# Performance work log

Hardware: AMD Instinct MI355X
Metric: run time of the kernel (lower is better)

The kernel has to match this reference:

```python
import jax, jax.numpy as jnp
import numpy as np

DIM = 768
HEADS = 12
HEAD_DIM = DIM // HEADS
SCALE = HEAD_DIM ** -0.5
ALPHA = 0.1


def setup_inputs() -> dict:
    key = jax.random.key(0)
    ks = jax.random.split(key, 6)
    B, N, C = 16, 577, DIM
    x = jax.random.normal(ks[0], (B, N, C), dtype=jnp.float32)
    attn_weight = jax.random.uniform(ks[1], (B, N - 1), dtype=jnp.float32)
    w_qkv = jax.random.normal(ks[2], (C, 3 * C), dtype=jnp.float32) * (C ** -0.5)
    b_qkv = jnp.zeros((3 * C,), dtype=jnp.float32)
    w_proj = jax.random.normal(ks[3], (C, C), dtype=jnp.float32) * (C ** -0.5)
    b_proj = jnp.zeros((C,), dtype=jnp.float32)
    return {"x": x, "attn_weight": attn_weight, "w_qkv": w_qkv, "b_qkv": b_qkv,
            "w_proj": w_proj, "b_proj": b_proj}


def reference(x, attn_weight, w_qkv, b_qkv, w_proj, b_proj):
    B, N, C = x.shape
    H, D = HEADS, HEAD_DIM
    qkv = (x @ w_qkv + b_qkv).reshape(B, N, 3, H, D)
    qkv = jnp.transpose(qkv, (2, 0, 3, 1, 4))  # [3, B, H, N, D]
    q, k, v = qkv[0], qkv[1], qkv[2]
    attn = jnp.einsum('bhnd,bhmd->bhnm', q, k) * SCALE  # [B,H,N,N]
    patch_attn = attn[:, :, 0, 1:]  # pre-softmax CLS->patch scores
    # reweight CLS row (excluding CLS->CLS) before softmax
    w = attn_weight[:, None, None, :]  # [B,1,1,N-1]
    cls_row = attn[:, :, 0:1, 1:] * (w * ALPHA + (1.0 - ALPHA))
    attn = attn.at[:, :, 0:1, 1:].set(cls_row)
    attn = jax.nn.softmax(attn, axis=-1)
    out = jnp.einsum('bhnm,bhmd->bhnd', attn, v)
    out = jnp.transpose(out, (0, 2, 1, 3)).reshape(B, N, C)
    out = out @ w_proj + b_proj
    return out, patch_attn
```

## Files before the change

kernel.cpp:

```cpp
#include <hip/hip_runtime.h>
#include <hip/hip_bf16.h>
#include <math.h>

#define B_    16
#define N_    577
#define C_    768
#define H_    12
#define D_    64
#define M_    (B_ * N_)
#define MP_   9344
#define QKVN  2304
#define NP_   640
#define SCALE 0.125f
#define ALPHA 0.1f
#define OUT0  (B_ * N_ * C_)

#define NB_CONV 7008
#define NB_T1   1728
#define NB_T2   576

typedef __attribute__((ext_vector_type(8))) short short8;
typedef __attribute__((ext_vector_type(4))) float f32x4;
typedef __hip_bfloat16 bf16;

__device__ __forceinline__ float exp2fast(float x) {
    return __builtin_amdgcn_exp2f(x);
}

__device__ __forceinline__ void load16(const void* g, void* l) {
    __builtin_amdgcn_global_load_lds(
        (const __attribute__((address_space(1))) unsigned int*)g,
        (__attribute__((address_space(3))) unsigned int*)l, 16, 0, 0);
}

__device__ __forceinline__ f32x4 mfma16(short8 a, short8 b, f32x4 c) {
    return __builtin_amdgcn_mfma_f32_16x16x32_bf16(a, b, c, 0, 0, 0);
}

#define FENCE() asm volatile("" ::: "memory")
#define BARRIER() do { FENCE(); __builtin_amdgcn_s_barrier(); FENCE(); } while (0)
#define WAITLGKM0() asm volatile("s_waitcnt lgkmcnt(0)" ::: "memory")

__global__ __launch_bounds__(256) void prep(const float* __restrict__ x,
                                            bf16* __restrict__ xb,
                                            const float* __restrict__ wq,
                                            bf16* __restrict__ wqT,
                                            const float* __restrict__ wp,
                                            bf16* __restrict__ wpT) {
    __shared__ float tile[32][33];
    const int bid = blockIdx.x;
    if (bid < NB_CONV) {
        int idx = bid * 256 + threadIdx.x;
        int m = idx / 192;
        bf16 tmp[4];
        if (m < M_) {
            float4 f = ((const float4*)x)[idx];
            tmp[0] = __float2bfloat16(f.x);
            tmp[1] = __float2bfloat16(f.y);
            tmp[2] = __float2bfloat16(f.z);
            tmp[3] = __float2bfloat16(f.w);
        } else {
            tmp[0] = tmp[1] = tmp[2] = tmp[3] = __float2bfloat16(0.f);
        }
        ((ushort4*)xb)[idx] = *(ushort4*)tmp;
        return;
    }
    const float* src; bf16* dst; int C, R, bx, by;
    if (bid < NB_CONV + NB_T1) {
        int r = bid - NB_CONV;
        bx = r % 72; by = r / 72; src = wq; dst = wqT; R = 768; C = QKVN;
    } else {
        int r = bid - NB_CONV - NB_T1;
        bx = r % 24; by = r / 24; src = wp; dst = wpT; R = 768; C = 768;
    }
    int cb = bx * 32, rb = by * 32;
    int tx = threadIdx.x & 31, ty = threadIdx.x >> 5;
    #pragma unroll
    for (int i = 0; i < 32; i += 8)
        tile[ty + i][tx] = src[(size_t)(rb + ty + i) * C + cb + tx];
    __syncthreads();
    #pragma unroll
    for (int i = 0; i < 32; i += 8)
        dst[(size_t)(cb + ty + i) * R + rb + tx] = __float2bfloat16(tile[tx][ty + i]);
}

__global__ __launch_bounds__(512, 2) void gemm256(const bf16* __restrict__ A,
                                                  const bf16* __restrict__ BT,
                                                  const float* __restrict__ bias,
                                                  bf16* __restrict__ q,
                                                  bf16* __restrict__ kk,
                                                  bf16* __restrict__ vt,
                                                  float* __restrict__ out,
                                                  int mode, int nby) {
    __shared__ __align__(16) char smem[131072];

    const int bid = blockIdx.x;
    const int mb = bid / nby;
    const int nb = bid % nby;
    const int m0 = mb * 256, n0 = nb * 256;
    const int t = threadIdx.x, lane = t & 63, w = t >> 6;
    const int wr = w >> 2, wc = w & 3;
    const int r16 = lane & 15, quad = lane >> 4;

    f32x4 acc[8][4];
    #pragma unroll
    for (int i = 0; i < 8; i++)
        #pragma unroll
        for (int j = 0; j < 4; j++) acc[i][j] = (f32x4)(0.f);

    const int lrow = lane >> 3;
    const int clog = ((lane & 7) ^ lrow) << 4;
    const int s2 = w * 2;
    const char* gA = (const char*)A  + (size_t)(m0 + lrow) * 1536 + clog;
    const char* gB = (const char*)BT + (size_t)(n0 + lrow) * 1536 + clog;

    auto stA = [&](int kt2, int half) {
        int ro = (half * 128 + s2 * 8) * 1536 + kt2 * 128;
        char* d = (char*)smem + (kt2 & 1) * 32768 + half * 16384 + s2 * 1024;
        load16(gA + ro, d);
        load16(gA + ro + 8 * 1536, d + 1024);
    };
    auto stB = [&](int kt2, int half) {
        int ro = (half * 128 + s2 * 8) * 1536 + kt2 * 128;
        char* d = (char*)smem + 65536 + (kt2 & 1) * 32768 + half * 16384 + s2 * 1024;
        load16(gB + ro, d);
        load16(gB + ro + 8 * 1536, d + 1024);
    };

    stA(0, 0); stA(0, 1); stB(0, 0); stB(0, 1);
    stA(1, 0); stA(1, 1);
    asm volatile("s_waitcnt vmcnt(4)" ::: "memory");
    BARRIER();

    const int sw = r16 & 7;
    const int g0 = (quad ^ sw) << 4;
    const int g1 = ((quad ^ 4) ^ sw) << 4;

    short8 af0[8], af1[8], bq0[2], bq1[2];

    #pragma unroll
    for (int kt = 0; kt < 12; kt++) {
        const int cur = kt & 1;
        const char* Ap = (const char*)smem + cur * 32768 + (wr * 128 + r16) * 128;
        const char* Bp = (const char*)smem + 65536 + cur * 32768 + (wc * 64 + r16) * 128;

        #pragma unroll
        for (int mi = 0; mi < 8; mi++) af0[mi] = *(const short8*)(Ap + mi * 2048 + g0);
        bq0[0] = *(const short8*)(Bp + 0 * 2048 + g0);
        bq0[1] = *(const short8*)(Bp + 1 * 2048 + g0);
        if (kt < 11) stB(kt + 1, 0);
        BARRIER();
        WAITLGKM0();
        __builtin_amdgcn_s_setprio(1);
        #pragma unroll
        for (int mi = 0; mi < 8; mi++) acc[mi][0] = mfma16(af0[mi], bq0[0], acc[mi][0]);
        #pragma unroll
        for (int mi = 0; mi < 8; mi++) acc[mi][1] = mfma16(af0[mi], bq0[1], acc[mi][1]);
        __builtin_amdgcn_s_setprio(0);
        BARRIER();

        #pragma unroll
        for (int mi = 0; mi < 8; mi++) af1[mi] = *(const short8*)(Ap + mi * 2048 + g1);
        bq1[0] = *(const short8*)(Bp + 2 * 2048 + g0);
        bq1[1] = *(const short8*)(Bp + 3 * 2048 + g0);
        if (kt < 11) stB(kt + 1, 1);
        BARRIER();
        WAITLGKM0();
        __builtin_amdgcn_s_setprio(1);
        #pragma unroll
        for (int mi = 0; mi < 8; mi++) acc[mi][2] = mfma16(af0[mi], bq1[0], acc[mi][2]);
        #pragma unroll
        for (int mi = 0; mi < 8; mi++) acc[mi][3] = mfma16(af0[mi], bq1[1], acc[mi][3]);
        __builtin_amdgcn_s_setprio(0);
        BARRIER();

        bq0[0] = *(const short8*)(Bp + 0 * 2048 + g1);
        bq0[1] = *(const short8*)(Bp + 1 * 2048 + g1);
        if (kt < 10) stA(kt + 2, 0);
        BARRIER();
        WAITLGKM0();
        __builtin_amdgcn_s_setprio(1);
        #pragma unroll
        for (int mi = 0; mi < 8; mi++) acc[mi][0] = mfma16(af1[mi], bq0[0], acc[mi][0]);
        #pragma unroll
        for (int mi = 0; mi < 8; mi++) acc[mi][1] = mfma16(af1[mi], bq0[1], acc[mi][1]);
        __builtin_amdgcn_s_setprio(0);
        BARRIER();

        bq1[0] = *(const short8*)(Bp + 2 * 2048 + g1);
        bq1[1] = *(const short8*)(Bp + 3 * 2048 + g1);
        if (kt < 10) stA(kt + 2, 1);
        BARRIER();
        WAITLGKM0();
        __builtin_amdgcn_s_setprio(1);
        #pragma unroll
        for (int mi = 0; mi < 8; mi++) acc[mi][2] = mfma16(af1[mi], bq1[0], acc[mi][2]);
        #pragma unroll
        for (int mi = 0; mi < 8; mi++) acc[mi][3] = mfma16(af1[mi], bq1[1], acc[mi][3]);
        __builtin_amdgcn_s_setprio(0);
        if (kt < 10) { asm volatile("s_waitcnt vmcnt(4)" ::: "memory"); }
        else         { asm volatile("s_waitcnt vmcnt(0)" ::: "memory"); }
        BARRIER();
    }

    float bs[4];
    #pragma unroll
    for (int nj = 0; nj < 4; nj++) bs[nj] = bias[n0 + wc * 64 + nj * 16 + r16];

    if (mode == 1) {
        #pragma unroll
        for (int mi = 0; mi < 8; mi++) {
            #pragma unroll
            for (int nj = 0; nj < 4; nj++) {
                #pragma unroll
                for (int r = 0; r < 4; r++) {
                    int m = m0 + wr * 128 + mi * 16 + quad * 4 + r;
                    if (m >= M_) continue;
                    out[(size_t)m * 768 + n0 + wc * 64 + nj * 16 + r16] = acc[mi][nj][r] + bs[nj];
                }
            }
        }
        return;
    }

    bf16* Tt = (bf16*)smem;
    const int part = nb / 3;
    const int h0 = (nb % 3) * 4;

    #pragma unroll
    for (int rh = 0; rh < 2; rh++) {
        __syncthreads();
        if (wr == rh) {
            #pragma unroll
            for (int mi = 0; mi < 8; mi++) {
                #pragma unroll
                for (int nj = 0; nj < 4; nj++) {
                    bf16 pk[4];
                    #pragma unroll
                    for (int r = 0; r < 4; r++)
                        pk[r] = __float2bfloat16(acc[mi][nj][r] + bs[nj]);
                    int ccl = wc * 64 + nj * 16 + r16;
                    int ml4 = mi * 16 + quad * 4;
                    *(uint2*)&Tt[ccl * 140 + ml4] = *(const uint2*)pk;
                }
            }
        }
        __syncthreads();
        if (part < 2) {
            int nl = t & 127, hq = t >> 7;
            int m = m0 + rh * 128 + nl;
            if (m < M_) {
                int b = m / N_, n = m - b * N_;
                bf16* dst = (part == 0 ? q : kk) + ((size_t)(b * H_ + h0 + hq) * N_ + n) * 64;
                #pragma unroll
                for (int d8 = 0; d8 < 8; d8++) {
                    bf16 tv[8];
                    #pragma unroll
                    for (int dd = 0; dd < 8; dd++)
                        tv[dd] = Tt[(hq * 64 + d8 * 8 + dd) * 140 + nl];
                    *(uint4*)(dst + d8 * 8) = *(const uint4*)tv;
                }
            }
        } else {
            int dr = t >> 1, seg = t & 1;
            int rem = (nb % 3) * 256 + dr;
            int h = rem >> 6, d = rem & 63;
            int mb2 = m0 + rh * 128 + seg * 64;
            int b = mb2 / N_;
            int n = mb2 - b * N_;
            const bf16* src = Tt + dr * 140 + seg * 64;
            int i = 0;
            while (i < 64 && mb2 + i < M_) {
                if (n == N_) { b++; n = 0; }
                bf16* drow = vt + ((size_t)(b * H_ + h) * 64 + d) * NP_;
                if ((n & 7) == 0 && n + 8 <= N_ && i + 8 <= 64 && mb2 + i + 8 <= M_) {
                    bf16 tv[8];
                    #pragma unroll
                    for (int dd = 0; dd < 8; dd++) tv[dd] = src[i + dd];
                    *(uint4*)(drow + n) = *(const uint4*)tv;
                    i += 8; n += 8;
                } else {
                    drow[n] = src[i]; i++; n++;
                }
            }
        }
    }
}

__global__ __launch_bounds__(256) void attn_mfma(const bf16* __restrict__ q,
                                                 const bf16* __restrict__ k,
                                                 const bf16* __restrict__ vt,
                                                 const float* __restrict__ aw,
                                                 bf16* __restrict__ ao,
                                                 float* __restrict__ patch) {
    __shared__ bf16 Kb[2][4096];
    __shared__ bf16 Vb[2][4096];
    __shared__ bf16 Pb[4][2048];
    const int bh = blockIdx.x, qt = blockIdx.y;
    const int b = bh / H_, h = bh - b * H_;
    const int t = threadIdx.x, lane = t & 63, w = t >> 6;
    const int r16 = lane & 15, quad = lane >> 4;
    const float SC2 = SCALE * 1.44269504f;

    const bf16* kbp = k + (size_t)bh * N_ * 64;
    const bf16* vbp = vt + (size_t)bh * 64 * NP_;

    short8 qa0[2], qa1[2];
    #pragma unroll
    for (int mi = 0; mi < 2; mi++) {
        int qrow = qt * 128 + w * 32 + mi * 16 + r16;
        int qrc = (qrow < N_) ? qrow : (N_ - 1);
        const bf16* qp = q + ((size_t)bh * N_ + qrc) * 64 + quad * 8;
        qa0[mi] = *(const short8*)(qp);
        qa1[mi] = *(const short8*)(qp + 32);
    }

    f32x4 Oacc[2][4];
    #pragma unroll
    for (int mi = 0; mi < 2; mi++)
        #pragma unroll
        for (int d0 = 0; d0 < 4; d0++) Oacc[mi][d0] = (f32x4)(0.f);
    float lrow[2][4];
    #pragma unroll
    for (int mi = 0; mi < 2; mi++)
        #pragma unroll
        for (int rr = 0; rr < 4; rr++) lrow[mi][rr] = 0.f;

    const bool clsrow = (qt == 0) && (w == 0) && (quad == 0);

    auto stage = [&](int kt, int buf) {
        #pragma unroll
        for (int is = 0; is < 2; is++) {
            int base = is * 256 + w * 64;
            int slot = base + lane;
            int row = slot >> 3, pos = slot & 7;
            int c = pos ^ (row & 7);
            int jg = kt * 64 + row; if (jg > N_ - 1) jg = N_ - 1;
            load16(kbp + (size_t)jg * 64 + c * 8, &Kb[buf][base * 8]);
        }
        #pragma unroll
        for (int is = 0; is < 2; is++) {
            int base = is * 256 + w * 64;
            int slot = base + lane;
            int row = slot >> 3, pos = slot & 7;
            int c = pos ^ (row & 7);
            load16(vbp + (size_t)row * NP_ + kt * 64 + c * 8, &Vb[buf][base * 8]);
        }
    };

    stage(0, 0);
    __syncthreads();

    for (int kt = 0; kt < 10; kt++) {
        const int cur = kt & 1;
        if (kt < 9) stage(kt + 1, cur ^ 1);

        f32x4 S[2][4];
        #pragma unroll
        for (int j0 = 0; j0 < 4; j0++) {
            int row = j0 * 16 + r16;
            const bf16* kpl = &Kb[cur][row * 64];
            short8 kf0 = *(const short8*)(kpl + ((quad ^ (row & 7)) << 3));
            short8 kf1 = *(const short8*)(kpl + (((quad ^ 4) ^ (row & 7)) << 3));
            #pragma unroll
            for (int mi = 0; mi < 2; mi++) {
                f32x4 sa = (f32x4)(0.f);
                sa = mfma16(qa0[mi], kf0, sa);
                sa = mfma16(qa1[mi], kf1, sa);
                S[mi][j0] = sa;
            }
        }

        if (kt < 9) {
            #pragma unroll
            for (int mi = 0; mi < 2; mi++) {
                #pragma unroll
                for (int j0 = 0; j0 < 4; j0++) {
                    float wfac = 1.f;
                    if (mi == 0 && clsrow) {
                        int c = kt * 64 + j0 * 16 + r16;
                        if (c >= 1) {
                            patch[(size_t)bh * (N_ - 1) + (c - 1)] = S[0][j0][0] * SCALE;
                            wfac = aw[b * (N_ - 1) + (c - 1)] * ALPHA + (1.f - ALPHA);
                        }
                    }
                    #pragma unroll
                    for (int rr = 0; rr < 4; rr++) {
                        float v = S[mi][j0][rr] * SC2;
                        if (rr == 0) v *= wfac;
                        float p = exp2fast(v);
                        S[mi][j0][rr] = p;
                        lrow[mi][rr] += p;
                    }
                }
            }
        } else {
            #pragma unroll
            for (int mi = 0; mi < 2; mi++) {
                #pragma unroll
                for (int j0 = 0; j0 < 4; j0++) {
                    int c = kt * 64 + j0 * 16 + r16;
                    bool valid = (c < N_);
                    float wfac = 1.f;
                    if (mi == 0 && clsrow && valid) {
                        patch[(size_t)bh * (N_ - 1) + (c - 1)] = S[0][j0][0] * SCALE;
                        wfac = aw[b * (N_ - 1) + (c - 1)] * ALPHA + (1.f - ALPHA);
                    }
                    #pragma unroll
                    for (int rr = 0; rr < 4; rr++) {
                        float v = S[mi][j0][rr] * SC2;
                        if (rr == 0) v *= wfac;
                        float p = valid ? exp2fast(v) : 0.f;
                        S[mi][j0][rr] = p;
                        lrow[mi][rr] += p;
                    }
                }
            }
        }

        bf16* pw = &Pb[w][0];
        #pragma unroll
        for (int mi = 0; mi < 2; mi++) {
            #pragma unroll
            for (int j0 = 0; j0 < 4; j0++) {
                int cg = j0 * 2 + (r16 >> 3);
                #pragma unroll
                for (int rr = 0; rr < 4; rr++) {
                    int rp = mi * 16 + quad * 4 + rr;
                    pw[rp * 64 + ((cg ^ (rp & 7)) << 3) + (r16 & 7)] =
                        __float2bfloat16(S[mi][j0][rr]);
                }
            }
        }
        short8 pa0[2], pa1[2];
        #pragma unroll
        for (int mi = 0; mi < 2; mi++) {
            int rp = mi * 16 + r16;
            const bf16* pr = pw + rp * 64;
            pa0[mi] = *(const short8*)(pr + ((quad ^ (rp & 7)) << 3));
            pa1[mi] = *(const short8*)(pr + (((quad ^ 4) ^ (rp & 7)) << 3));
        }

        #pragma unroll
        for (int d0 = 0; d0 < 4; d0++) {
            int row = d0 * 16 + r16;
            const bf16* vpl = &Vb[cur][row * 64];
            short8 vf0 = *(const short8*)(vpl + ((quad ^ (row & 7)) << 3));
            short8 vf1 = *(const short8*)(vpl + (((quad ^ 4) ^ (row & 7)) << 3));
            #pragma unroll
            for (int mi = 0; mi < 2; mi++) {
                Oacc[mi][d0] = mfma16(pa0[mi], vf0, Oacc[mi][d0]);
                Oacc[mi][d0] = mfma16(pa1[mi], vf1, Oacc[mi][d0]);
            }
        }
        __syncthreads();
    }

    #pragma unroll
    for (int mi = 0; mi < 2; mi++) {
        #pragma unroll
        for (int rr = 0; rr < 4; rr++) {
            float l = lrow[mi][rr];
            l += __shfl_xor(l, 1);
            l += __shfl_xor(l, 2);
            l += __shfl_xor(l, 4);
            l += __shfl_xor(l, 8);
            int n = qt * 128 + w * 32 + mi * 16 + quad * 4 + rr;
            if (n >= N_) continue;
            float inv = 1.f / l;
            #pragma unroll
            for (int d0 = 0; d0 < 4; d0++) {
                ao[((size_t)(b * N_ + n) * H_ + h) * 64 + d0 * 16 + r16] =
                    __float2bfloat16(Oacc[mi][d0][rr] * inv);
            }
        }
    }
}

extern "C" void kernel_launch(void* const* d_in, const int* in_sizes, int n_in,
                              void* d_out, int out_size, void* d_ws, size_t ws_size,
                              hipStream_t stream) {
    const float* x      = (const float*)d_in[0];
    const float* aw     = (const float*)d_in[1];
    const float* w_qkv  = (const float*)d_in[2];
    const float* b_qkv  = (const float*)d_in[3];
    const float* w_proj = (const float*)d_in[4];
    const float* b_proj = (const float*)d_in[5];
    float* out = (float*)d_out;

    char* ws = (char*)d_ws;
    bf16* xbf    = (bf16*)(ws);
    bf16* wqkvT  = (bf16*)(ws + 14352384);
    bf16* wprojT = (bf16*)(ws + 17891328);
    bf16* qv     = (bf16*)(ws + 19070976);
    bf16* kv     = (bf16*)(ws + 33251328);
    bf16* vt     = (bf16*)(ws + 47431680);
    bf16* ao     = xbf;

    prep<<<NB_CONV + NB_T1 + NB_T2, 256, 0, stream>>>(x, xbf, w_qkv, wqkvT, w_proj, wprojT);

    gemm256<<<37 * 9, 512, 0, stream>>>(
        xbf, wqkvT, b_qkv, qv, kv, vt, nullptr, 0, 9);

    attn_mfma<<<dim3(H_ * B_, 5), 256, 0, stream>>>(qv, kv, vt, aw, ao, out + OUT0);

    gemm256<<<37 * 3, 512, 0, stream>>>(
        ao, wprojT, b_proj, nullptr, nullptr, nullptr, out, 1, 3);
}
```

Measured before the change: 229.3 us.

## Remap GEMM workgroups per XCD and restage A/B tiles together per k-step

The bf16 MFMA GEMM now remaps block IDs so consecutive tiles land on the same XCD, which should improve L2 reuse of shared A/B panels. The K loop is restructured: each k-tile issues one combined global-to-LDS stage of both A and B for tile k+2, after the last fragment read rather than interleaved between compute phases. Fragments are now loaded as 4x4 A/B groups instead of 8x2, and the loop is only partially unrolled in pairs with explicit vmcnt waits. This lowers register pressure and code size but makes each prefetch burst larger and later, with less overlap with compute.

Result: slower. 238.8 us (+4.1%).

```diff
diff --git a/kernel.cpp b/kernel.cpp
--- a/kernel.cpp
+++ b/kernel.cpp
@@ -94,9 +94,13 @@
                                                   int mode, int nby) {
     __shared__ __align__(16) char smem[131072];
 
-    const int bid = blockIdx.x;
-    const int mb = bid / nby;
-    const int nb = bid % nby;
+    const int nwg = gridDim.x;
+    const int orig = blockIdx.x;
+    const int xcd = orig & 7, ii = orig >> 3;
+    const int qq = nwg >> 3, rr = nwg & 7;
+    const int wg = (xcd < rr ? xcd * (qq + 1) : rr * (qq + 1) + (xcd - rr) * qq) + ii;
+    const int mb = wg / nby;
+    const int nb = wg - mb * nby;
     const int m0 = mb * 256, n0 = nb * 256;
     const int t = threadIdx.x, lane = t & 63, w = t >> 6;
     const int wr = w >> 2, wc = w & 3;
@@ -114,94 +118,103 @@
     const char* gA = (const char*)A  + (size_t)(m0 + lrow) * 1536 + clog;
     const char* gB = (const char*)BT + (size_t)(n0 + lrow) * 1536 + clog;
 
-    auto stA = [&](int kt2, int half) {
-        int ro = (half * 128 + s2 * 8) * 1536 + kt2 * 128;
-        char* d = (char*)smem + (kt2 & 1) * 32768 + half * 16384 + s2 * 1024;
-        load16(gA + ro, d);
-        load16(gA + ro + 8 * 1536, d + 1024);
+    auto stage = [&](int kt2) {
+        const int bo = (kt2 & 1) * 32768;
+        const int kc = kt2 * 128;
+        #pragma unroll
+        for (int half = 0; half < 2; half++) {
+            int ro = (half * 128 + s2 * 8) * 1536 + kc;
+            char* dA = (char*)smem + bo + half * 16384 + s2 * 1024;
+            char* dB = dA + 65536;
+            load16(gA + ro, dA);
+            load16(gA + ro + 8 * 1536, dA + 1024);
+            load16(gB + ro, dB);
+            load16(gB + ro + 8 * 1536, dB + 1024);
+        }
     };
-    auto stB = [&](int kt2, int half) {
-        int ro = (half * 128 + s2 * 8) * 1536 + kt2 * 128;
-        char* d = (char*)smem + 65536 + (kt2 & 1) * 32768 + half * 16384 + s2 * 1024;
-        load16(gB + ro, d);
-        load16(gB + ro + 8 * 1536, d + 1024);
-    };
-
-    stA(0, 0); stA(0, 1); stB(0, 0); stB(0, 1);
-    stA(1, 0); stA(1, 1);
-    asm volatile("s_waitcnt vmcnt(4)" ::: "memory");
+
+    stage(0);
+    stage(1);
+    asm volatile("s_waitcnt vmcnt(8)" ::: "memory");
     BARRIER();
 
     const int sw = r16 & 7;
     const int g0 = (quad ^ sw) << 4;
     const int g1 = ((quad ^ 4) ^ sw) << 4;
 
-    short8 af0[8], af1[8], bq0[2], bq1[2];
-
-    #pragma unroll
-    for (int kt = 0; kt < 12; kt++) {
-        const int cur = kt & 1;
+    auto tile = [&](int k, bool doStage, int vmN) {
+        const int cur = k & 1;
         const char* Ap = (const char*)smem + cur * 32768 + (wr * 128 + r16) * 128;
         const char* Bp = (const char*)smem + 65536 + cur * 32768 + (wc * 64 + r16) * 128;
-
-        #pragma unroll
-        for (int mi = 0; mi < 8; mi++) af0[mi] = *(const short8*)(Ap + mi * 2048 + g0);
-        bq0[0] = *(const short8*)(Bp + 0 * 2048 + g0);
-        bq0[1] = *(const short8*)(Bp + 1 * 2048 + g0);
-        if (kt < 11) stB(kt + 1, 0);
+        short8 af[4], bf[4];
+
+        #pragma unroll
+        for (int mi = 0; mi < 4; mi++) af[mi] = *(const short8*)(Ap + mi * 2048 + g0);
+        #pragma unroll
+        for (int nj = 0; nj < 4; nj++) bf[nj] = *(const short8*)(Bp + nj * 2048 + g0);
         BARRIER();
         WAITLGKM0();
         __builtin_amdgcn_s_setprio(1);
         #pragma unroll
-        for (int mi = 0; mi < 8; mi++) acc[mi][0] = mfma16(af0[mi], bq0[0], acc[mi][0]);
-        #pragma unroll
-        for (int mi = 0; mi < 8; mi++) acc[mi][1] = mfma16(af0[mi], bq0[1], acc[mi][1]);
+        for (int mi = 0; mi < 4; mi++)
+            #pragma unroll
+            for (int nj = 0; nj < 4; nj++)
+                acc[mi][nj] = mfma16(af[mi], bf[nj], acc[mi][nj]);
         __builtin_amdgcn_s_setprio(0);
         BARRIER();
 
         #pragma unroll
-        for (int mi = 0; mi < 8; mi++) af1[mi] = *(const short8*)(Ap + mi * 2048 + g1);
-        bq1[0] = *(const short8*)(Bp + 2 * 2048 + g0);
-        bq1[1] = *(const short8*)(Bp + 3 * 2048 + g0);
-        if (kt < 11) stB(kt + 1, 1);
+        for (int mi = 0; mi < 4; mi++) af[mi] = *(const short8*)(Ap + (mi + 4) * 2048 + g0);
         BARRIER();
         WAITLGKM0();
         __builtin_amdgcn_s_setprio(1);
         #pragma unroll
-        for (int mi = 0; mi < 8; mi++) acc[mi][2] = mfma16(af0[mi], bq1[0], acc[mi][2]);
-        #pragma unroll
-        for (int mi = 0; mi < 8; mi++) acc[mi][3] = mfma16(af0[mi], bq1[1], acc[mi][3]);
+        for (int mi = 0; mi < 4; mi++)
+            #pragma unroll
+            for (int nj = 0; nj < 4; nj++)
+                acc[mi + 4][nj] = mfma16(af[mi], bf[nj], acc[mi + 4][nj]);
         __builtin_amdgcn_s_setprio(0);
         BARRIER();
 
-        bq0[0] = *(const short8*)(Bp + 0 * 2048 + g1);
-        bq0[1] = *(const short8*)(Bp + 1 * 2048 + g1);
-        if (kt < 10) stA(kt + 2, 0);
+        #pragma unroll
+        for (int mi = 0; mi < 4; mi++) af[mi] = *(const short8*)(Ap + mi * 2048 + g1);
+        #pragma unroll
+        for (int nj = 0; nj < 4; nj++) bf[nj] = *(const short8*)(Bp + nj * 2048 + g1);
         BARRIER();
         WAITLGKM0();
         __builtin_amdgcn_s_setprio(1);
         #pragma unroll
-        for (int mi = 0; mi < 8; mi++) acc[mi][0] = mfma16(af1[mi], bq0[0], acc[mi][0]);
-        #pragma unroll
-        for (int mi = 0; mi < 8; mi++) acc[mi][1] = mfma16(af1[mi], bq0[1], acc[mi][1]);
+        for (int mi = 0; mi < 4; mi++)
+            #pragma unroll
+            for (int nj = 0; nj < 4; nj++)
+                acc[mi][nj] = mfma16(af[mi], bf[nj], acc[mi][nj]);
         __builtin_amdgcn_s_setprio(0);
         BARRIER();
 
-        bq1[0] = *(const short8*)(Bp + 2 * 2048 + g1);
-        bq1[1] = *(const short8*)(Bp + 3 * 2048 + g1);
-        if (kt < 10) stA(kt + 2, 1);
+        #pragma unroll
+        for (int mi = 0; mi < 4; mi++) af[mi] = *(const short8*)(Ap + (mi + 4) * 2048 + g1);
         BARRIER();
         WAITLGKM0();
+        if (doStage) stage(k + 2);
         __builtin_amdgcn_s_setprio(1);
         #pragma unroll
-        for (int mi = 0; mi < 8; mi++) acc[mi][2] = mfma16(af1[mi], bq1[0], acc[mi][2]);
-        #pragma unroll
-        for (int mi = 0; mi < 8; mi++) acc[mi][3] = mfma16(af1[mi], bq1[1], acc[mi][3]);
+        for (int mi = 0; mi < 4; mi++)
+            #pragma unroll
+            for (int nj = 0; nj < 4; nj++)
+                acc[mi + 4][nj] = mfma16(af[mi], bf[nj], acc[mi + 4][nj]);
         __builtin_amdgcn_s_setprio(0);
-        if (kt < 10) { asm volatile("s_waitcnt vmcnt(4)" ::: "memory"); }
-        else         { asm volatile("s_waitcnt vmcnt(0)" ::: "memory"); }
-        BARRIER();
-    }
+        if (vmN == 8)      { asm volatile("s_waitcnt vmcnt(8)" ::: "memory"); }
+        else if (vmN == 0) { asm volatile("s_waitcnt vmcnt(0)" ::: "memory"); }
+        BARRIER();
+    };
+
+    #pragma unroll 1
+    for (int kp = 0; kp < 5; kp++) {
+        tile(2 * kp,     true, 8);
+        tile(2 * kp + 1, true, 8);
+    }
+    tile(10, false, 0);
+    tile(11, false, -1);
 
     float bs[4];
     #pragma unroll
```
